# Performance work log

Hardware: AMD Instinct MI355X
Metric: run time of the kernel (lower is better)

The kernel has to match this reference:

```python
import math
import jax, jax.numpy as jnp
import numpy as np

NUM_COEFFS = 64
REPEAT = 4
IN_CH = 256
OUT_CH = 256
BATCH = 8
SEQ_L = 8192


def setup_inputs() -> dict:
    key = jax.random.key(0)
    k1, k2 = jax.random.split(key)
    n = NUM_COEFFS * REPEAT
    # S4D-style init, exactly as in the torch __init__
    log_A_real = np.log(np.exp(0.5) - 1.0) * np.ones(NUM_COEFFS)
    A_imag = math.pi * np.arange(NUM_COEFFS)
    A = np.tile(np.stack([log_A_real, A_imag], -1), (REPEAT, 1))  # [n, 2]
    B = np.ones((n, IN_CH)) / math.sqrt(IN_CH)                    # [n, c_in]
    log_dt = np.repeat(np.linspace(np.log(0.001), np.log(0.1), REPEAT), NUM_COEFFS)  # [n]
    C = jax.random.normal(k1, (OUT_CH, n), dtype=jnp.float32) * math.sqrt(2.0 / n)
    x = jax.random.normal(k2, (BATCH, IN_CH, SEQ_L), dtype=jnp.float32)
    return {
        "x": x,
        "A": jnp.asarray(A, dtype=jnp.float32),
        "B": jnp.asarray(B, dtype=jnp.float32),
        "log_dt": jnp.asarray(log_dt, dtype=jnp.float32),
        "C": C,
    }


def _fft_conv_bnl(x, K):
    # Causal/linear convolution via zero-padded FFT of length 2L, keep first L.
    # x: [b, n, l], K: [n, l] -> [b, n, l]
    l = x.shape[-1]
    xf = jnp.fft.rfft(x, 2 * l)
    kf = jnp.fft.rfft(K, 2 * l)
    y = jnp.fft.irfft(xf * kf, 2 * l)
    return y[..., :l]


def reference(x, A, B, log_dt, C):
    L = x.shape[-1]
    # ssm_basis_kernels
    log_A_real, A_imag = A[:, 0], A[:, 1]          # [n]
    lrange = jnp.arange(L, dtype=x.dtype)          # [L]
    dt = jnp.exp(log_dt)                           # [n]
    dtA_real = -dt * jax.nn.softplus(log_A_real)
    dtA_imag = dt * A_imag
    K = jnp.exp(dtA_real[:, None] * lrange) * jnp.cos(dtA_imag[:, None] * lrange)  # [n, L]
    B_hat = B * dt[:, None]                        # [n, c_in]
    # opt_ssm_forward: with these shapes the torch code takes the coeffs<=c_in branch
    xb = jnp.einsum('bcl,nc->bnl', x, B_hat)       # project into state basis
    y = _fft_conv_bnl(xb, K)                       # per-state long conv via FFT
    return jnp.einsum('bnl,dn->bdl', y, C)         # project to output channels
```

## Files before the change

### kernel.cpp

```cpp
#include <hip/hip_runtime.h>
#include <hip/hip_bf16.h>
#include <math.h>

#define BATCH 8
#define L_SEQ 8192
#define KD    256

typedef __attribute__((ext_vector_type(8))) short bf16x8;
typedef __attribute__((ext_vector_type(4))) float f32x4;

__device__ __forceinline__ void async_ld16(const __hip_bfloat16* g, __hip_bfloat16* l) {
    __builtin_amdgcn_global_load_lds(
        (const __attribute__((address_space(1))) unsigned int*)g,
        (__attribute__((address_space(3))) unsigned int*)l, 16, 0, 0);
}

__global__ void prep(const float* __restrict__ B, const float* __restrict__ logdt,
                     const float* __restrict__ C, const float* __restrict__ A,
                     __hip_bfloat16* __restrict__ W1bf, __hip_bfloat16* __restrict__ Cbf,
                     float2* __restrict__ lamtab) {
    int i = blockIdx.x * 256 + threadIdx.x;
    W1bf[i] = __float2bfloat16(B[i] * expf(logdt[i >> 8]));
    Cbf[i]  = __float2bfloat16(C[i]);
    if (blockIdx.x == 0) {
        int n = threadIdx.x;
        float dt  = expf(logdt[n]);
        float dAr = -dt * log1pf(expf(A[2 * n]));
        float dAi = dt * A[2 * n + 1];
        float e1 = expf(dAr);
        lamtab[n * 4 + 0] = make_float2(e1 * cosf(dAi), e1 * sinf(dAi));
        float e16 = expf(16.f * dAr);
        lamtab[n * 4 + 1] = make_float2(e16 * cosf(16.f * dAi), e16 * sinf(16.f * dAi));
        float e128 = expf(128.f * dAr);
        lamtab[n * 4 + 2] = make_float2(e128 * cosf(128.f * dAi), e128 * sinf(128.f * dAi));
        lamtab[n * 4 + 3] = make_float2(dAr, dAi);
    }
}

__global__ __launch_bounds__(256) void gemm1(
        const float* __restrict__ X, const __hip_bfloat16* __restrict__ W1,
        const float2* __restrict__ lamtab,
        __hip_bfloat16* __restrict__ XBT, float2* __restrict__ sums)
{
    __shared__ __hip_bfloat16 Abuf[16 * 512];
    __shared__ __hip_bfloat16 Bbuf[16 * 512];

    const int t = threadIdx.x, lane = t & 63, wave = t >> 6;
    const int wr = wave >> 1, wc = wave & 1;
    const int lm = lane & 15, lq = lane >> 4;
    const int seg = blockIdx.y;
    const int row0 = seg * 128;
    const int col0 = blockIdx.x * 128;
    const int b = blockIdx.z;
    const float* Xb = X + (size_t)b * KD * L_SEQ;

    const int c8  = t >> 5;
    const int l4  = (t & 31) * 4;
    const int s_w = c8 >> 2;
    const int lq_w = c8 & 3;

    f32x4 acc[4][4];
#pragma unroll
    for (int i = 0; i < 4; ++i)
#pragma unroll
        for (int j = 0; j < 4; ++j) acc[i][j] = {0.f, 0.f, 0.f, 0.f};

    for (int k0 = 0; k0 < KD; k0 += 64) {
#pragma unroll
        for (int i = 0; i < 4; ++i) {
            int jb = wave * 4 + i, ct = jb >> 1, sB = jb & 1;
            const __hip_bfloat16* g =
                W1 + (size_t)(col0 + ct * 16 + lm) * KD + k0 + sB * 32 + lq * 8;
            async_ld16(g, &Bbuf[jb * 512 + lane * 8]);
        }
        float4 xv[8];
#pragma unroll
        for (int i = 0; i < 8; ++i)
            xv[i] = *(const float4*)(Xb + (size_t)(k0 + c8 * 8 + i) * L_SEQ + row0 + l4);
#pragma unroll
        for (int j = 0; j < 4; ++j) {
            int l = l4 + j;
            int rt = l >> 4, lmW = l & 15;
            union { __hip_bfloat16 h[8]; uint4 u; } pk;
#pragma unroll
            for (int i = 0; i < 8; ++i) {
                const float* f = (const float*)&xv[i];
                pk.h[i] = __float2bfloat16(f[j]);
            }
            int slot = (lmW ^ rt ^ (s_w << 3)) + 16 * lq_w;
            *(uint4*)&Abuf[(rt * 2 + s_w) * 512 + slot * 8] = pk.u;
        }
        __syncthreads();
#pragma unroll
        for (int s = 0; s < 2; ++s) {
            bf16x8 af[4], bfr[4];
#pragma unroll
            for (int i = 0; i < 4; ++i) {
                int rt = wr * 4 + i;
                int slot = (lm ^ rt ^ (s << 3)) + 16 * lq;
                af[i] = *(const bf16x8*)&Abuf[(rt * 2 + s) * 512 + slot * 8];
            }
#pragma unroll
            for (int j = 0; j < 4; ++j)
                bfr[j] = *(const bf16x8*)&Bbuf[((wc * 4 + j) * 2 + s) * 512 + lane * 8];
#pragma unroll
            for (int i = 0; i < 4; ++i)
#pragma unroll
                for (int j = 0; j < 4; ++j)
                    acc[i][j] = __builtin_amdgcn_mfma_f32_16x16x32_bf16(
                        af[i], bfr[j], acc[i][j], 0, 0, 0);
        }
        __syncthreads();
    }

    __hip_bfloat16* Db = XBT + (size_t)b * L_SEQ * KD;
#pragma unroll
    for (int i = 0; i < 4; ++i) {
        int r0 = row0 + wr * 64 + i * 16 + lq * 4;
#pragma unroll
        for (int j = 0; j < 4; ++j) {
            int c = col0 + wc * 64 + j * 16 + lm;
#pragma unroll
            for (int r = 0; r < 4; ++r)
                Db[(size_t)(r0 + r) * KD + c] = __float2bfloat16(acc[i][j][r]);
        }
    }

    float2 par[4];
#pragma unroll
    for (int j = 0; j < 4; ++j) {
        int n = col0 + wc * 64 + j * 16 + lm;
        float2 dA  = lamtab[n * 4 + 3];
        float2 lam = lamtab[n * 4 + 0];
        float m1r = lam.x, m1i = lam.y;
        float sr = 0.f, si = 0.f;
#pragma unroll
        for (int i = 0; i < 4; ++i) {
            int lbase = wr * 64 + i * 16 + lq * 4;
            float p = (float)(127 - lbase - 3);
            float er = expf(dA.x * p);
            float wrr = er * cosf(dA.y * p), wii = er * sinf(dA.y * p);
            for (int r = 3; r >= 0; --r) {
                float v = acc[i][j][r];
                sr += wrr * v; si += wii * v;
                float nr = wrr * m1r - wii * m1i;
                float ni = wrr * m1i + wii * m1r;
                wrr = nr; wii = ni;
            }
        }
        sr += __shfl_xor(sr, 16); si += __shfl_xor(si, 16);
        sr += __shfl_xor(sr, 32); si += __shfl_xor(si, 32);
        par[j] = make_float2(sr, si);
    }
    float2* ssum = (float2*)Bbuf;
    if (wr == 0 && lq == 0) {
#pragma unroll
        for (int j = 0; j < 4; ++j) ssum[wc * 64 + j * 16 + lm] = par[j];
    }
    __syncthreads();
    if (wr == 1 && lq == 0) {
#pragma unroll
        for (int j = 0; j < 4; ++j) {
            float2 o = ssum[wc * 64 + j * 16 + lm];
            int n = col0 + wc * 64 + j * 16 + lm;
            sums[((size_t)b * KD + n) * 64 + seg] =
                make_float2(par[j].x + o.x, par[j].y + o.y);
        }
    }
}

__global__ __launch_bounds__(64) void scan_carry(
        const float2* __restrict__ lamtab, float2* __restrict__ sums) {
    const int lane = threadIdx.x;
    const int b = blockIdx.x >> 8, n = blockIdx.x & 255;
    float2 m = lamtab[n * 4 + 2];
    float mr = m.x, mi = m.y;
    float2 s = sums[((size_t)b * KD + n) * 64 + lane];
    float vr = s.x, vi = s.y;
#pragma unroll
    for (int d = 1; d < 64; d <<= 1) {
        float ur = __shfl_up(vr, (unsigned)d);
        float ui = __shfl_up(vi, (unsigned)d);
        if (lane >= d) {
            float tr = mr * ur - mi * ui + vr;
            float ti = mr * ui + mi * ur + vi;
            vr = tr; vi = ti;
        }
        float m2r = mr * mr - mi * mi;
        float m2i = 2.0f * mr * mi;
        mr = m2r; mi = m2i;
    }
    float cr = __shfl_up(vr, 1u), ci = __shfl_up(vi, 1u);
    if (lane == 0) { cr = 0.f; ci = 0.f; }
    sums[((size_t)b * KD + n) * 64 + lane] = make_float2(cr, ci);
}

__global__ __launch_bounds__(256) void scan_apply(
        __hip_bfloat16* __restrict__ XBT, const float2* __restrict__ lamtab,
        const float2* __restrict__ sums)
{
    __shared__ float2 sl[8][258];
    const int t = threadIdx.x;
    const int sub = t >> 5, n0 = (t & 31) * 8;
    const int seg = blockIdx.x, b = blockIdx.y;
    __hip_bfloat16* base = XBT + ((size_t)b * L_SEQ + seg * 128 + sub * 16) * KD + n0;

    float2 lam[8];
#pragma unroll
    for (int k = 0; k < 8; ++k) lam[k] = lamtab[(n0 + k) * 4];

    uint4 xv[16];
    float sr[8], si[8];
#pragma unroll
    for (int k = 0; k < 8; ++k) { sr[k] = 0.f; si[k] = 0.f; }

#pragma unroll
    for (int l = 0; l < 16; ++l) {
        xv[l] = *(const uint4*)(base + (size_t)l * KD);
        const __hip_bfloat16* xs = (const __hip_bfloat16*)&xv[l];
#pragma unroll
        for (int k = 0; k < 8; ++k) {
            float v = __bfloat162float(xs[k]);
            float nr = lam[k].x * sr[k] - lam[k].y * si[k] + v;
            float ni = lam[k].x * si[k] + lam[k].y * sr[k];
            sr[k] = nr; si[k] = ni;
        }
    }
#pragma unroll
    for (int k = 0; k < 8; ++k) sl[sub][n0 + k] = make_float2(sr[k], si[k]);
    __syncthreads();

    {
        int n = t;
        float2 m16 = lamtab[n * 4 + 1];
        float2 c = sums[((size_t)b * KD + n) * 64 + seg];
        float cr = c.x, ci = c.y;
#pragma unroll
        for (int s2 = 0; s2 < 8; ++s2) {
            float2 loc = sl[s2][n];
            sl[s2][n] = make_float2(cr, ci);
            float nr = m16.x * cr - m16.y * ci + loc.x;
            float ni = m16.x * ci + m16.y * cr + loc.y;
            cr = nr; ci = ni;
        }
    }
    __syncthreads();

#pragma unroll
    for (int k = 0; k < 8; ++k) {
        float2 c = sl[sub][n0 + k];
        sr[k] = c.x; si[k] = c.y;
    }
#pragma unroll
    for (int l = 0; l < 16; ++l) {
        const __hip_bfloat16* xs = (const __hip_bfloat16*)&xv[l];
        union { __hip_bfloat16 h[8]; uint4 u; } yv;
#pragma unroll
        for (int k = 0; k < 8; ++k) {
            float v = __bfloat162float(xs[k]);
            float nr = lam[k].x * sr[k] - lam[k].y * si[k] + v;
            float ni = lam[k].x * si[k] + lam[k].y * sr[k];
            sr[k] = nr; si[k] = ni;
            yv.h[k] = __float2bfloat16(nr);
        }
        *(uint4*)(base + (size_t)l * KD) = yv.u;
    }
}

__global__ __launch_bounds__(256) void gemm2(
        const __hip_bfloat16* __restrict__ Ag,
        const __hip_bfloat16* __restrict__ Bg,
        float* __restrict__ Dg)
{
    const int t = threadIdx.x, lane = t & 63, wave = t >> 6;
    const int wr = wave >> 1, wc = wave & 1;
    const int row0 = blockIdx.y * 128, col0 = blockIdx.x * 128;
    const int lm = lane & 15, lq = lane >> 4;
    const __hip_bfloat16* Bb = Bg + (size_t)blockIdx.z * L_SEQ * KD;
    float* Db = Dg + (size_t)blockIdx.z * KD * L_SEQ;

    const __hip_bfloat16* Ab  = Ag + (size_t)(row0 + wr * 64 + lm) * KD + lq * 8;
    const __hip_bfloat16* Bbp = Bb + (size_t)(col0 + wc * 64 + lm) * KD + lq * 8;

    f32x4 acc[4][4];
#pragma unroll
    for (int i = 0; i < 4; ++i)
#pragma unroll
        for (int j = 0; j < 4; ++j) acc[i][j] = {0.f, 0.f, 0.f, 0.f};

#pragma unroll
    for (int kt = 0; kt < 4; ++kt) {
        bf16x8 af[2][4], bfr[2][4];
#pragma unroll
        for (int s = 0; s < 2; ++s)
#pragma unroll
            for (int i = 0; i < 4; ++i) {
                af[s][i]  = *(const bf16x8*)(Ab  + (size_t)(i * 16) * KD + kt * 64 + s * 32);
                bfr[s][i] = *(const bf16x8*)(Bbp + (size_t)(i * 16) * KD + kt * 64 + s * 32);
            }
#pragma unroll
        for (int s = 0; s < 2; ++s)
#pragma unroll
            for (int i = 0; i < 4; ++i)
#pragma unroll
                for (int j = 0; j < 4; ++j)
                    acc[i][j] = __builtin_amdgcn_mfma_f32_16x16x32_bf16(
                        af[s][i], bfr[s][j], acc[i][j], 0, 0, 0);
    }

#pragma unroll
    for (int i = 0; i < 4; ++i) {
        int r0 = row0 + wr * 64 + i * 16 + lq * 4;
#pragma unroll
        for (int j = 0; j < 4; ++j) {
            int c = col0 + wc * 64 + j * 16 + lm;
#pragma unroll
            for (int r = 0; r < 4; ++r)
                Db[(size_t)(r0 + r) * L_SEQ + c] = acc[i][j][r];
        }
    }
}

extern "C" void kernel_launch(void* const* d_in, const int* in_sizes, int n_in,
                              void* d_out, int out_size, void* d_ws, size_t ws_size,
                              hipStream_t stream) {
    const float* x      = (const float*)d_in[0];
    const float* A      = (const float*)d_in[1];
    const float* B      = (const float*)d_in[2];
    const float* log_dt = (const float*)d_in[3];
    const float* C      = (const float*)d_in[4];
    float* out = (float*)d_out;

    char* ws = (char*)d_ws;
    __hip_bfloat16* W1bf = (__hip_bfloat16*)(ws);
    __hip_bfloat16* Cbf  = (__hip_bfloat16*)(ws + (128 << 10));
    float2*         lamtab = (float2*)(ws + (256 << 10));
    float2*         sums = (float2*)(ws + (320 << 10));
    __hip_bfloat16* xb_t = (__hip_bfloat16*)(ws + ((size_t)2 << 20));

    prep<<<256, 256, 0, stream>>>(B, log_dt, C, A, W1bf, Cbf, lamtab);
    gemm1<<<dim3(2, 64, BATCH), 256, 0, stream>>>(x, W1bf, lamtab, xb_t, sums);
    scan_carry<<<BATCH * KD, 64, 0, stream>>>(lamtab, sums);
    scan_apply<<<dim3(64, BATCH), 256, 0, stream>>>(xb_t, lamtab, sums);
    gemm2<<<dim3(L_SEQ / 128, KD / 128, BATCH), 256, 0, stream>>>(Cbf, xb_t, out);
}
```

Measured before the change: 191.9 us.

## Fuse scan-apply into output GEMM via swizzled LDS staging

Merges the scan_apply and gemm2 kernels into one. Each block recomputes the scanned state for its 128-position segment, writes the bf16 results into a swizzled 64KB LDS buffer, and then runs the C projection MFMA directly from LDS. This drops the global write and reread of the scanned intermediate and one kernel launch. In exchange, the scan for each segment is recomputed twice, once per output-row tile, and the large LDS footprint lowers occupancy.

```diff
diff --git a/kernel.cpp b/kernel.cpp
--- a/kernel.cpp
+++ b/kernel.cpp
@@ -195,15 +195,23 @@
     sums[((size_t)b * KD + n) * 64 + lane] = make_float2(cr, ci);
 }
 
-__global__ __launch_bounds__(256) void scan_apply(
-        __hip_bfloat16* __restrict__ XBT, const float2* __restrict__ lamtab,
-        const float2* __restrict__ sums)
+__global__ __launch_bounds__(256) void scan_gemm2(
+        const __hip_bfloat16* __restrict__ XBT,
+        const float2* __restrict__ lamtab,
+        const float2* __restrict__ sums,
+        const __hip_bfloat16* __restrict__ Ag,
+        float* __restrict__ Dg)
 {
-    __shared__ float2 sl[8][258];
+    __shared__ __align__(16) char lds_raw[65536];
+    __hip_bfloat16 (*Ybuf)[16 * 512] = (__hip_bfloat16 (*)[16 * 512])lds_raw;
+    float2 (*sl)[258] = (float2 (*)[258])lds_raw;
+
     const int t = threadIdx.x;
+    const int seg = blockIdx.x, dtile = blockIdx.y, b = blockIdx.z;
     const int sub = t >> 5, n0 = (t & 31) * 8;
-    const int seg = blockIdx.x, b = blockIdx.y;
-    __hip_bfloat16* base = XBT + ((size_t)b * L_SEQ + seg * 128 + sub * 16) * KD + n0;
+
+    const __hip_bfloat16* base =
+        XBT + ((size_t)b * L_SEQ + seg * 128 + sub * 16) * KD + n0;
 
     float2 lam[8];
 #pragma unroll
@@ -251,36 +259,34 @@
         float2 c = sl[sub][n0 + k];
         sr[k] = c.x; si[k] = c.y;
     }
-#pragma unroll
-    for (int l = 0; l < 16; ++l) {
-        const __hip_bfloat16* xs = (const __hip_bfloat16*)&xv[l];
-        union { __hip_bfloat16 h[8]; uint4 u; } yv;
-#pragma unroll
-        for (int k = 0; k < 8; ++k) {
-            float v = __bfloat162float(xs[k]);
-            float nr = lam[k].x * sr[k] - lam[k].y * si[k] + v;
-            float ni = lam[k].x * si[k] + lam[k].y * sr[k];
-            sr[k] = nr; si[k] = ni;
-            yv.h[k] = __float2bfloat16(nr);
-        }
-        *(uint4*)(base + (size_t)l * KD) = yv.u;
-    }
-}
-
-__global__ __launch_bounds__(256) void gemm2(
-        const __hip_bfloat16* __restrict__ Ag,
-        const __hip_bfloat16* __restrict__ Bg,
-        float* __restrict__ Dg)
-{
-    const int t = threadIdx.x, lane = t & 63, wave = t >> 6;
+    __syncthreads();
+
+    {
+        const int kt_w = n0 >> 6, s_w = (n0 >> 5) & 1, lq_w = (n0 >> 3) & 3;
+#pragma unroll
+        for (int l = 0; l < 16; ++l) {
+            const __hip_bfloat16* xs = (const __hip_bfloat16*)&xv[l];
+            union { __hip_bfloat16 h[8]; uint4 u; } yv;
+#pragma unroll
+            for (int k = 0; k < 8; ++k) {
+                float v = __bfloat162float(xs[k]);
+                float nr = lam[k].x * sr[k] - lam[k].y * si[k] + v;
+                float ni = lam[k].x * si[k] + lam[k].y * sr[k];
+                sr[k] = nr; si[k] = ni;
+                yv.h[k] = __float2bfloat16(nr);
+            }
+            int slotS = lq_w * 16 + (l ^ lq_w ^ (s_w << 2));
+            *(uint4*)&Ybuf[kt_w][(sub * 2 + s_w) * 512 + slotS * 8] = yv.u;
+        }
+    }
+    __syncthreads();
+
+    const int lane = t & 63, wave = t >> 6;
     const int wr = wave >> 1, wc = wave & 1;
-    const int row0 = blockIdx.y * 128, col0 = blockIdx.x * 128;
     const int lm = lane & 15, lq = lane >> 4;
-    const __hip_bfloat16* Bb = Bg + (size_t)blockIdx.z * L_SEQ * KD;
-    float* Db = Dg + (size_t)blockIdx.z * KD * L_SEQ;
-
-    const __hip_bfloat16* Ab  = Ag + (size_t)(row0 + wr * 64 + lm) * KD + lq * 8;
-    const __hip_bfloat16* Bbp = Bb + (size_t)(col0 + wc * 64 + lm) * KD + lq * 8;
+    const int row0 = dtile * 128, col0 = seg * 128;
+    const __hip_bfloat16* Ab = Ag + (size_t)(row0 + wr * 64 + lm) * KD + lq * 8;
+    float* Db = Dg + (size_t)b * KD * L_SEQ;
 
     f32x4 acc[4][4];
 #pragma unroll
@@ -290,22 +296,23 @@
 
 #pragma unroll
     for (int kt = 0; kt < 4; ++kt) {
-        bf16x8 af[2][4], bfr[2][4];
-#pragma unroll
-        for (int s = 0; s < 2; ++s)
-#pragma unroll
-            for (int i = 0; i < 4; ++i) {
-                af[s][i]  = *(const bf16x8*)(Ab  + (size_t)(i * 16) * KD + kt * 64 + s * 32);
-                bfr[s][i] = *(const bf16x8*)(Bbp + (size_t)(i * 16) * KD + kt * 64 + s * 32);
-            }
-#pragma unroll
-        for (int s = 0; s < 2; ++s)
+#pragma unroll
+        for (int s = 0; s < 2; ++s) {
+            bf16x8 af[4], bfr[4];
+#pragma unroll
+            for (int i = 0; i < 4; ++i)
+                af[i] = *(const bf16x8*)(Ab + (size_t)(i * 16) * KD + kt * 64 + s * 32);
+            int slotS = lq * 16 + (lm ^ lq ^ (s << 2));
+#pragma unroll
+            for (int j = 0; j < 4; ++j)
+                bfr[j] = *(const bf16x8*)&Ybuf[kt][((wc * 4 + j) * 2 + s) * 512 + slotS * 8];
 #pragma unroll
             for (int i = 0; i < 4; ++i)
 #pragma unroll
                 for (int j = 0; j < 4; ++j)
                     acc[i][j] = __builtin_amdgcn_mfma_f32_16x16x32_bf16(
-                        af[s][i], bfr[s][j], acc[i][j], 0, 0, 0);
+                        af[i], bfr[j], acc[i][j], 0, 0, 0);
+        }
     }
 
 #pragma unroll
@@ -341,6 +348,5 @@
     prep<<<256, 256, 0, stream>>>(B, log_dt, C, A, W1bf, Cbf, lamtab);
     gemm1<<<dim3(2, 64, BATCH), 256, 0, stream>>>(x, W1bf, lamtab, xb_t, sums);
     scan_carry<<<BATCH * KD, 64, 0, stream>>>(lamtab, sums);
-    scan_apply<<<dim3(64, BATCH), 256, 0, stream>>>(xb_t, lamtab, sums);
-    gemm2<<<dim3(L_SEQ / 128, KD / 128, BATCH), 256, 0, stream>>>(Cbf, xb_t, out);
-}
+    scan_gemm2<<<dim3(64, 2, BATCH), 256, 0, stream>>>(xb_t, lamtab, sums, Cbf, out);
+}
```

Measured after the change: 189.2 us. Within noise of the previous version (-1.4%).
